# Kernel optimization log

Measured on AMD Instinct MI355X. Metric: run time of the kernel, lower is better.

The kernel has to match this reference:

```python
import jax, jax.numpy as jnp
import numpy as np

N_EXPERTS = 8
IN_DIM = 1024
OUT_DIM = 1024
N_TOKENS = 16384
TOP_K = 2


def setup_inputs() -> dict:
    key = jax.random.key(0)
    k1, k2, k3, k4 = jax.random.split(key, 4)
    inputs = jax.random.normal(k1, (N_TOKENS, IN_DIM), dtype=jnp.float32)
    # weight stored as [n_experts, out_dim, in_dim] like the nn.Parameter
    weight = jax.random.normal(k2, (N_EXPERTS, OUT_DIM, IN_DIM), dtype=jnp.float32) * 0.02
    gates = jax.random.uniform(k3, (N_TOKENS, TOP_K), dtype=jnp.float32)
    # router assignments: each token gets TOP_K expert ids; slots sorted by expert
    expert_idxs = jax.random.randint(k4, (N_TOKENS, TOP_K), 0, N_EXPERTS)
    flat = expert_idxs.reshape(-1)                       # [n_tokens*k]
    sorted_scattered_idxs = jnp.argsort(flat).astype(jnp.int64)
    sorted_expert_idxs = flat[sorted_scattered_idxs].astype(jnp.int64)
    expert_offsets = jnp.cumsum(jnp.bincount(flat, length=N_EXPERTS)).astype(jnp.int64)
    return {
        "inputs": inputs,
        "weight": weight,
        "gates": gates,
        "k": TOP_K,
        "sorted_expert_idxs": sorted_expert_idxs,
        "sorted_scattered_idxs": sorted_scattered_idxs,
        "expert_offsets": expert_offsets,
    }


def reference(inputs, weight, gates, k, sorted_expert_idxs, sorted_scattered_idxs, expert_offsets):
    # scatter2scatter (grouped_in=False, grouped_out=False, bias=None):
    #   slot j uses expert e=sorted_expert_idxs[j] on token t=sorted_scattered_idxs[j]//k
    #   slot_out[j] = weight[e] @ x[t]   (weight passed as W.permute(0,2,1), same math)
    tok = sorted_scattered_idxs // k                      # [S]
    xs = jnp.take(inputs, tok, axis=0)                    # [S, Din] gathered in sorted order
    S = xs.shape[0]
    n_experts, out_dim = weight.shape[0], weight.shape[1]
    slot_out = jnp.zeros((S, out_dim), dtype=xs.dtype)
    for e in range(n_experts):                            # small fixed expert count
        mask = (sorted_expert_idxs == e)[:, None].astype(xs.dtype)
        slot_out = slot_out + (xs * mask) @ weight[e].T   # [S, Dout]
    # gate-weighted combine, faithful to the torch code: the sorted slot
    # output is viewed directly as [n_tokens, k, out_dim]
    n_tokens, kk = gates.shape
    out_expanded = slot_out.reshape(n_tokens, kk, out_dim)
    return jnp.einsum('tk,tko->to', gates, out_expanded)  # [n_tokens, out_dim]
```

## Files before the change

### kernel.cpp

```cpp
#include <hip/hip_runtime.h>
#include <stdint.h>

#define N_EXPERTS 8
#define IN_DIM    1024
#define OUT_DIM   1024
#define N_TOKENS  16384
#define S_SLOTS   (N_TOKENS * 2)
#define BM 128
#define BN 128
#define BK 32
#define MAX_TILES 264

typedef unsigned short u16;
using short4v = __attribute__((ext_vector_type(4))) short;
using short8  = __attribute__((ext_vector_type(8))) short;
using f32x4   = __attribute__((ext_vector_type(4))) float;

__device__ __forceinline__ u16 f2bf(float f) {
  uint32_t x = __builtin_bit_cast(uint32_t, f);
  uint32_t r = x + 0x7fffu + ((x >> 16) & 1u);
  return (u16)(r >> 16);
}
__device__ __forceinline__ float bf2f(u16 u) {
  uint32_t x = ((uint32_t)u) << 16;
  return __builtin_bit_cast(float, x);
}

#define GLD_LDS16(g, l) __builtin_amdgcn_global_load_lds(            \
    (const __attribute__((address_space(1))) void*)(g),              \
    (__attribute__((address_space(3))) void*)(l), 16, 0, 0)

__global__ __launch_bounds__(256) void convert_two(
    const float* __restrict__ X, const float* __restrict__ W,
    u16* __restrict__ Xb, u16* __restrict__ Wb, int xblocks, int xn8, int wn8) {
  const float* src; u16* dst; int i, n8;
  if ((int)blockIdx.x < xblocks) {
    i = blockIdx.x * 256 + threadIdx.x; src = X; dst = Xb; n8 = xn8;
  } else {
    i = (blockIdx.x - xblocks) * 256 + threadIdx.x; src = W; dst = Wb; n8 = wn8;
  }
  if (i >= n8) return;
  const f32x4* s = (const f32x4*)src + (size_t)i * 2;
  f32x4 v0 = s[0], v1 = s[1];
  short8 o;
#pragma unroll
  for (int j = 0; j < 4; ++j) {
    o[j]     = (short)f2bf(v0[j]);
    o[4 + j] = (short)f2bf(v1[j]);
  }
  *(short8*)(dst + (size_t)i * 8) = o;
}

__device__ __forceinline__ bool derive_tile(const int* eoff_raw, bool is64,
                                            int bx, int& expert, int& rs, int& re) {
  int rem = bx, prev = 0;
  expert = -1;
  for (int e = 0; e < N_EXPERTS; ++e) {
    int end = is64 ? eoff_raw[2 * e] : eoff_raw[e];
    int cnt = end - prev;
    int nt  = (cnt + BM - 1) / BM;
    if (expert < 0) {
      if (rem < nt) {
        expert = e;
        rs = prev + rem * BM;
        re = (rs + BM < end) ? (rs + BM) : end;
      } else {
        rem -= nt;
      }
    }
    prev = end;
  }
  return expert >= 0;
}

__global__ __launch_bounds__(256) void moe_gemm_slot(
    const u16* __restrict__ Xb,
    const u16* __restrict__ Wb,
    const int* __restrict__ kptr,
    const int* __restrict__ ssi_raw,
    const int* __restrict__ eoff_raw,
    u16*       __restrict__ slot_out)
{
  __shared__ __align__(16) u16 smem[BM * BN];
  u16* As = smem;
  u16* Bs = smem + BM * BK;

  const bool is64 = (eoff_raw[7] != S_SLOTS);
  int expert, rs, re;
  if (!derive_tile(eoff_raw, is64, blockIdx.x, expert, rs, re)) return;
  const int rcount = re - rs;

  const int n0   = blockIdx.y * BN;
  const int kdiv = kptr[0];
  const int t    = threadIdx.x;

  const int r0 = t >> 2;
  const int r1 = (t + 256) >> 2;
  const int cg = (t & 3) * 8;

  int g0 = rs + r0; if (g0 >= re) g0 = re - 1;
  int g1 = rs + r1; if (g1 >= re) g1 = re - 1;
  const int tok0 = (is64 ? ssi_raw[2 * g0] : ssi_raw[g0]) / kdiv;
  const int tok1 = (is64 ? ssi_raw[2 * g1] : ssi_raw[g1]) / kdiv;

  const u16* a0 = Xb + (size_t)tok0 * IN_DIM + cg;
  const u16* a1 = Xb + (size_t)tok1 * IN_DIM + cg;
  const u16* wbp = Wb + (size_t)expert * OUT_DIM * IN_DIM;
  const u16* b0 = wbp + (size_t)(n0 + r0) * IN_DIM + cg;
  const u16* b1 = wbp + (size_t)(n0 + r1) * IN_DIM + cg;

  f32x4 acc[4][4];
#pragma unroll
  for (int i = 0; i < 4; ++i)
#pragma unroll
    for (int j = 0; j < 4; ++j)
      acc[i][j] = (f32x4){0.f, 0.f, 0.f, 0.f};

  const int wave = t >> 6;
  const int lane = t & 63;
  const int wm = (wave >> 1) * 64;
  const int wn = (wave & 1) * 64;
  const int lr = lane & 15;
  const int lk = (lane >> 4) * 8;

  for (int k0 = 0; k0 < IN_DIM; k0 += BK) {
    GLD_LDS16(a0 + k0, As + (size_t)t * 8);
    GLD_LDS16(a1 + k0, As + (size_t)(t + 256) * 8);
    GLD_LDS16(b0 + k0, Bs + (size_t)t * 8);
    GLD_LDS16(b1 + k0, Bs + (size_t)(t + 256) * 8);
    __syncthreads();

    short8 af[4], bfv[4];
#pragma unroll
    for (int mi = 0; mi < 4; ++mi)
      af[mi] = *(const short8*)&As[(wm + mi * 16 + lr) * BK + lk];
#pragma unroll
    for (int ni = 0; ni < 4; ++ni)
      bfv[ni] = *(const short8*)&Bs[(wn + ni * 16 + lr) * BK + lk];

#pragma unroll
    for (int mi = 0; mi < 4; ++mi)
#pragma unroll
      for (int ni = 0; ni < 4; ++ni)
        acc[mi][ni] = __builtin_amdgcn_mfma_f32_16x16x32_bf16(
            af[mi], bfv[ni], acc[mi][ni], 0, 0, 0);

    __syncthreads();
  }

  u16* Cs = smem;
#pragma unroll
  for (int mi = 0; mi < 4; ++mi)
#pragma unroll
    for (int ni = 0; ni < 4; ++ni)
#pragma unroll
      for (int r = 0; r < 4; ++r) {
        int row = wm + mi * 16 + (lane >> 4) * 4 + r;
        int col = wn + ni * 16 + lr;
        Cs[row * BN + col] = f2bf(acc[mi][ni][r]);
      }
  __syncthreads();

  const int crow = t >> 4;
  const int ccol = (t & 15) * 8;
#pragma unroll
  for (int i = 0; i < 8; ++i) {
    int row = i * 16 + crow;
    if (row < rcount) {
      *(short8*)&slot_out[(size_t)(rs + row) * OUT_DIM + n0 + ccol] =
          *(const short8*)&Cs[row * BN + ccol];
    }
  }
}

__global__ __launch_bounds__(256) void combine_k(
    const u16*   __restrict__ slot_out,
    const float* __restrict__ gates,
    float*       __restrict__ out)
{
  int idx = blockIdx.x * 256 + threadIdx.x;
  if (idx >= N_TOKENS * OUT_DIM / 8) return;
  int tk = idx >> 7;
  int cc = (idx & 127) * 8;
  float ga = gates[2 * tk];
  float gb = gates[2 * tk + 1];
  short8 s0 = *(const short8*)&slot_out[(size_t)(2 * tk) * OUT_DIM + cc];
  short8 s1 = *(const short8*)&slot_out[(size_t)(2 * tk + 1) * OUT_DIM + cc];
  f32x4 o0, o1;
#pragma unroll
  for (int j = 0; j < 4; ++j) {
    o0[j] = ga * bf2f((u16)s0[j])     + gb * bf2f((u16)s1[j]);
    o1[j] = ga * bf2f((u16)s0[4 + j]) + gb * bf2f((u16)s1[4 + j]);
  }
  f32x4* dst = (f32x4*)(out + (size_t)tk * OUT_DIM + cc);
  dst[0] = o0; dst[1] = o1;
}

__global__ __launch_bounds__(256) void moe_gemm_bf16(
    const u16*   __restrict__ Xb, const u16* __restrict__ Wb,
    const float* __restrict__ gates, const int* __restrict__ kptr,
    const int*   __restrict__ ssi_raw, const int* __restrict__ eoff_raw,
    float*       __restrict__ out)
{
  __shared__ __align__(16) u16 As[BM * BK];
  __shared__ __align__(16) u16 Bs[BN * BK];

  const bool is64 = (eoff_raw[7] != S_SLOTS);
  int expert, rs, re;
  if (!derive_tile(eoff_raw, is64, blockIdx.x, expert, rs, re)) return;
  const int rcount = re - rs;

  const int n0   = blockIdx.y * BN;
  const int kdiv = kptr[0];
  const int t    = threadIdx.x;

  const int r0 = t >> 2;
  const int r1 = (t + 256) >> 2;
  const int cg = (t & 3) * 8;

  int g0 = rs + r0; if (g0 >= re) g0 = re - 1;
  int g1 = rs + r1; if (g1 >= re) g1 = re - 1;
  const int tok0 = (is64 ? ssi_raw[2 * g0] : ssi_raw[g0]) / kdiv;
  const int tok1 = (is64 ? ssi_raw[2 * g1] : ssi_raw[g1]) / kdiv;

  const u16* a0 = Xb + (size_t)tok0 * IN_DIM + cg;
  const u16* a1 = Xb + (size_t)tok1 * IN_DIM + cg;
  const u16* wbp = Wb + (size_t)expert * OUT_DIM * IN_DIM;
  const u16* b0 = wbp + (size_t)(n0 + r0) * IN_DIM + cg;
  const u16* b1 = wbp + (size_t)(n0 + r1) * IN_DIM + cg;

  f32x4 acc[4][4];
#pragma unroll
  for (int i = 0; i < 4; ++i)
#pragma unroll
    for (int j = 0; j < 4; ++j)
      acc[i][j] = (f32x4){0.f, 0.f, 0.f, 0.f};

  const int wave = t >> 6;
  const int lane = t & 63;
  const int wm = (wave >> 1) * 64;
  const int wn = (wave & 1) * 64;
  const int lr = lane & 15;
  const int lk = (lane >> 4) * 8;

  for (int k0 = 0; k0 < IN_DIM; k0 += BK) {
    GLD_LDS16(a0 + k0, As + (size_t)t * 8);
    GLD_LDS16(a1 + k0, As + (size_t)(t + 256) * 8);
    GLD_LDS16(b0 + k0, Bs + (size_t)t * 8);
    GLD_LDS16(b1 + k0, Bs + (size_t)(t + 256) * 8);
    __syncthreads();

    short8 af[4], bfv[4];
#pragma unroll
    for (int mi = 0; mi < 4; ++mi)
      af[mi] = *(const short8*)&As[(wm + mi * 16 + lr) * BK + lk];
#pragma unroll
    for (int ni = 0; ni < 4; ++ni)
      bfv[ni] = *(const short8*)&Bs[(wn + ni * 16 + lr) * BK + lk];

#pragma unroll
    for (int mi = 0; mi < 4; ++mi)
#pragma unroll
      for (int ni = 0; ni < 4; ++ni)
        acc[mi][ni] = __builtin_amdgcn_mfma_f32_16x16x32_bf16(
            af[mi], bfv[ni], acc[mi][ni], 0, 0, 0);

    __syncthreads();
  }

#pragma unroll
  for (int mi = 0; mi < 4; ++mi) {
#pragma unroll
    for (int r = 0; r < 4; ++r) {
      int row = wm + mi * 16 + (lane >> 4) * 4 + r;
      if (row < rcount) {
        int slot  = rs + row;
        int token = slot / kdiv;
        float g   = gates[slot];
        float* dst = out + (size_t)token * OUT_DIM + n0;
#pragma unroll
        for (int ni = 0; ni < 4; ++ni) {
          int col = wn + ni * 16 + lr;
          atomicAdd(dst + col, g * acc[mi][ni][r]);
        }
      }
    }
  }
}

__global__ __launch_bounds__(256) void moe_gemm_fused(
    const float* __restrict__ X, const float* __restrict__ W,
    const float* __restrict__ gates, const int* __restrict__ kptr,
    const int*   __restrict__ ssi_raw, const int* __restrict__ eoff_raw,
    float*       __restrict__ out)
{
  __shared__ __align__(16) u16 As[BM * BK];
  __shared__ __align__(16) u16 Bs[BN * BK];

  const bool is64 = (eoff_raw[7] != S_SLOTS);
  int expert, rs, re;
  if (!derive_tile(eoff_raw, is64, blockIdx.x, expert, rs, re)) return;
  const int rcount = re - rs;

  const int n0   = blockIdx.y * BN;
  const int kdiv = kptr[0];
  const int t    = threadIdx.x;

  const float* arow[4];
  const float* brow[4];
  int lofs[4];
#pragma unroll
  for (int i = 0; i < 4; ++i) {
    int c = t + 256 * i;
    int r = c >> 3;
    int col4 = (c & 7) * 4;
    int g = rs + r; if (g >= re) g = re - 1;
    int sval = is64 ? ssi_raw[2 * g] : ssi_raw[g];
    int tok  = sval / kdiv;
    arow[i] = X + (size_t)tok * IN_DIM + col4;
    brow[i] = W + ((size_t)expert * OUT_DIM + n0 + r) * IN_DIM + col4;
    lofs[i] = r * BK + col4;
  }

  f32x4 acc[4][4];
#pragma unroll
  for (int i = 0; i < 4; ++i)
#pragma unroll
    for (int j = 0; j < 4; ++j)
      acc[i][j] = (f32x4){0.f, 0.f, 0.f, 0.f};

  const int wave = t >> 6;
  const int lane = t & 63;
  const int wm = (wave >> 1) * 64;
  const int wn = (wave & 1) * 64;
  const int lr = lane & 15;
  const int lk = (lane >> 4) * 8;

  for (int k0 = 0; k0 < IN_DIM; k0 += BK) {
    f32x4 a[4], b[4];
#pragma unroll
    for (int i = 0; i < 4; ++i) {
      a[i] = *(const f32x4*)(arow[i] + k0);
      b[i] = *(const f32x4*)(brow[i] + k0);
    }
    __syncthreads();
#pragma unroll
    for (int i = 0; i < 4; ++i) {
      short4v av, bv;
#pragma unroll
      for (int j = 0; j < 4; ++j) {
        av[j] = (short)f2bf(a[i][j]);
        bv[j] = (short)f2bf(b[i][j]);
      }
      *(short4v*)&As[lofs[i]] = av;
      *(short4v*)&Bs[lofs[i]] = bv;
    }
    __syncthreads();

    short8 af[4], bfv[4];
#pragma unroll
    for (int mi = 0; mi < 4; ++mi)
      af[mi] = *(const short8*)&As[(wm + mi * 16 + lr) * BK + lk];
#pragma unroll
    for (int ni = 0; ni < 4; ++ni)
      bfv[ni] = *(const short8*)&Bs[(wn + ni * 16 + lr) * BK + lk];

#pragma unroll
    for (int mi = 0; mi < 4; ++mi)
#pragma unroll
      for (int ni = 0; ni < 4; ++ni)
        acc[mi][ni] = __builtin_amdgcn_mfma_f32_16x16x32_bf16(
            af[mi], bfv[ni], acc[mi][ni], 0, 0, 0);
  }

#pragma unroll
  for (int mi = 0; mi < 4; ++mi) {
#pragma unroll
    for (int r = 0; r < 4; ++r) {
      int row = wm + mi * 16 + (lane >> 4) * 4 + r;
      if (row < rcount) {
        int slot  = rs + row;
        int token = slot / kdiv;
        float g   = gates[slot];
        float* dst = out + (size_t)token * OUT_DIM + n0;
#pragma unroll
        for (int ni = 0; ni < 4; ++ni) {
          int col = wn + ni * 16 + lr;
          atomicAdd(dst + col, g * acc[mi][ni][r]);
        }
      }
    }
  }
}

extern "C" void kernel_launch(void* const* d_in, const int* in_sizes, int n_in,
                              void* d_out, int out_size, void* d_ws, size_t ws_size,
                              hipStream_t stream) {
  const float* X     = (const float*)d_in[0];
  const float* W     = (const float*)d_in[1];
  const float* gates = (const float*)d_in[2];
  const int*   kptr  = (const int*)d_in[3];
  const int*   ssi   = (const int*)d_in[5];
  const int*   eoff  = (const int*)d_in[6];
  float* out = (float*)d_out;

  const size_t x_elems = (size_t)N_TOKENS * IN_DIM;
  const size_t w_elems = (size_t)N_EXPERTS * OUT_DIM * IN_DIM;
  const size_t s_elems = (size_t)S_SLOTS * OUT_DIM;
  const size_t need_full = (x_elems + w_elems + s_elems) * sizeof(u16);
  const size_t need_conv = (x_elems + w_elems) * sizeof(u16);

  const int xn8 = (int)(x_elems / 8), wn8 = (int)(w_elems / 8);
  const int xblocks = (xn8 + 255) / 256, wblocks = (wn8 + 255) / 256;

  if (ws_size >= need_full) {
    u16* Xb = (u16*)d_ws;
    u16* Wb = Xb + x_elems;
    u16* slot_out = Wb + w_elems;
    hipLaunchKernelGGL(convert_two, dim3(xblocks + wblocks), dim3(256), 0,
                       stream, X, W, Xb, Wb, xblocks, xn8, wn8);
    hipLaunchKernelGGL(moe_gemm_slot, dim3(MAX_TILES, OUT_DIM / BN), dim3(256),
                       0, stream, Xb, Wb, kptr, ssi, eoff, slot_out);
    const int nchunks = N_TOKENS * OUT_DIM / 8;
    hipLaunchKernelGGL(combine_k, dim3(nchunks / 256), dim3(256), 0, stream,
                       slot_out, gates, out);
  } else if (ws_size >= need_conv) {
    u16* Xb = (u16*)d_ws;
    u16* Wb = Xb + x_elems;
    hipMemsetAsync(d_out, 0, (size_t)out_size * sizeof(float), stream);
    hipLaunchKernelGGL(convert_two, dim3(xblocks + wblocks), dim3(256), 0,
                       stream, X, W, Xb, Wb, xblocks, xn8, wn8);
    hipLaunchKernelGGL(moe_gemm_bf16, dim3(MAX_TILES, OUT_DIM / BN), dim3(256),
                       0, stream, Xb, Wb, gates, kptr, ssi, eoff, out);
  } else {
    hipMemsetAsync(d_out, 0, (size_t)out_size * sizeof(float), stream);
    hipLaunchKernelGGL(moe_gemm_fused, dim3(MAX_TILES, OUT_DIM / BN), dim3(256),
                       0, stream, X, W, gates, kptr, ssi, eoff, out);
  }
}
```

Measured before the change: 260.5 us.

## Fuse convert, GEMM and combine into one persistent cooperative kernel

Replaces the three-kernel pipeline (bf16 conversion, slot GEMM, gated combine) with a single persistent cooperative kernel that uses grid-wide syncs between phases. GEMM tiles are handed out as jobs in a grid-stride loop. The aim is to remove kernel launch gaps and per-launch tail effects. In exchange it pays for two grid barriers, and the GEMM phase is limited to the blocks that can be co-resident (capped at 1056). It falls back to the old three-kernel path if the cooperative launch fails, and it drops the atomic bf16 path.

Result: slower. 433.3 us (+66.3%).

```diff
diff --git a/kernel.cpp b/kernel.cpp
--- a/kernel.cpp
+++ b/kernel.cpp
@@ -1,5 +1,8 @@
 #include <hip/hip_runtime.h>
+#include <hip/hip_cooperative_groups.h>
 #include <stdint.h>
+
+namespace cg = cooperative_groups;
 
 #define N_EXPERTS 8
 #define IN_DIM    1024
@@ -10,6 +13,7 @@
 #define BN 128
 #define BK 32
 #define MAX_TILES 264
+#define NGROUPS   (OUT_DIM / BN)
 
 typedef unsigned short u16;
 using short4v = __attribute__((ext_vector_type(4))) short;
@@ -29,27 +33,6 @@
 #define GLD_LDS16(g, l) __builtin_amdgcn_global_load_lds(            \
     (const __attribute__((address_space(1))) void*)(g),              \
     (__attribute__((address_space(3))) void*)(l), 16, 0, 0)
-
-__global__ __launch_bounds__(256) void convert_two(
-    const float* __restrict__ X, const float* __restrict__ W,
-    u16* __restrict__ Xb, u16* __restrict__ Wb, int xblocks, int xn8, int wn8) {
-  const float* src; u16* dst; int i, n8;
-  if ((int)blockIdx.x < xblocks) {
-    i = blockIdx.x * 256 + threadIdx.x; src = X; dst = Xb; n8 = xn8;
-  } else {
-    i = (blockIdx.x - xblocks) * 256 + threadIdx.x; src = W; dst = Wb; n8 = wn8;
-  }
-  if (i >= n8) return;
-  const f32x4* s = (const f32x4*)src + (size_t)i * 2;
-  f32x4 v0 = s[0], v1 = s[1];
-  short8 o;
-#pragma unroll
-  for (int j = 0; j < 4; ++j) {
-    o[j]     = (short)f2bf(v0[j]);
-    o[4 + j] = (short)f2bf(v1[j]);
-  }
-  *(short8*)(dst + (size_t)i * 8) = o;
-}
 
 __device__ __forceinline__ bool derive_tile(const int* eoff_raw, bool is64,
                                             int bx, int& expert, int& rs, int& re) {
@@ -73,48 +56,59 @@
   return expert >= 0;
 }
 
-__global__ __launch_bounds__(256) void moe_gemm_slot(
-    const u16* __restrict__ Xb,
-    const u16* __restrict__ Wb,
-    const int* __restrict__ kptr,
-    const int* __restrict__ ssi_raw,
-    const int* __restrict__ eoff_raw,
-    u16*       __restrict__ slot_out)
+__global__ __launch_bounds__(256, 4) void moe_fused(
+    const float* __restrict__ X,
+    const float* __restrict__ W,
+    const float* __restrict__ gates,
+    const int*   __restrict__ kptr,
+    const int*   __restrict__ ssi_raw,
+    const int*   __restrict__ eoff_raw,
+    u16* __restrict__ Xb, u16* __restrict__ Wb,
+    u16* __restrict__ slot_out,
+    float* __restrict__ out,
+    int nblk)
 {
   __shared__ __align__(16) u16 smem[BM * BN];
+  cg::grid_group grid = cg::this_grid();
+
+  const int bid = blockIdx.x;
+  const int t   = threadIdx.x;
+
+  const int xn8  = (N_TOKENS * IN_DIM) / 8;
+  const int wn8  = (N_EXPERTS * OUT_DIM * IN_DIM) / 8;
+  const int tot8 = xn8 + wn8;
+  for (int i = bid * 256 + t; i < tot8; i += nblk * 256) {
+    const float* src; u16* dst; int j;
+    if (i < xn8) { src = X; dst = Xb; j = i; }
+    else         { src = W; dst = Wb; j = i - xn8; }
+    f32x4 v0 = ((const f32x4*)src)[(size_t)j * 2];
+    f32x4 v1 = ((const f32x4*)src)[(size_t)j * 2 + 1];
+    short8 o;
+#pragma unroll
+    for (int q = 0; q < 4; ++q) {
+      o[q]     = (short)f2bf(v0[q]);
+      o[4 + q] = (short)f2bf(v1[q]);
+    }
+    *(short8*)(dst + (size_t)j * 8) = o;
+  }
+
+  grid.sync();
+
+  const bool is64 = (eoff_raw[7] != S_SLOTS);
+  int ntiles = 0;
+  {
+    int prev = 0;
+    for (int e = 0; e < N_EXPERTS; ++e) {
+      int end = is64 ? eoff_raw[2 * e] : eoff_raw[e];
+      ntiles += (end - prev + BM - 1) / BM;
+      prev = end;
+    }
+  }
+  const int njobs = ntiles * NGROUPS;
+  const int kdiv  = kptr[0];
+
   u16* As = smem;
   u16* Bs = smem + BM * BK;
-
-  const bool is64 = (eoff_raw[7] != S_SLOTS);
-  int expert, rs, re;
-  if (!derive_tile(eoff_raw, is64, blockIdx.x, expert, rs, re)) return;
-  const int rcount = re - rs;
-
-  const int n0   = blockIdx.y * BN;
-  const int kdiv = kptr[0];
-  const int t    = threadIdx.x;
-
-  const int r0 = t >> 2;
-  const int r1 = (t + 256) >> 2;
-  const int cg = (t & 3) * 8;
-
-  int g0 = rs + r0; if (g0 >= re) g0 = re - 1;
-  int g1 = rs + r1; if (g1 >= re) g1 = re - 1;
-  const int tok0 = (is64 ? ssi_raw[2 * g0] : ssi_raw[g0]) / kdiv;
-  const int tok1 = (is64 ? ssi_raw[2 * g1] : ssi_raw[g1]) / kdiv;
-
-  const u16* a0 = Xb + (size_t)tok0 * IN_DIM + cg;
-  const u16* a1 = Xb + (size_t)tok1 * IN_DIM + cg;
-  const u16* wbp = Wb + (size_t)expert * OUT_DIM * IN_DIM;
-  const u16* b0 = wbp + (size_t)(n0 + r0) * IN_DIM + cg;
-  const u16* b1 = wbp + (size_t)(n0 + r1) * IN_DIM + cg;
-
-  f32x4 acc[4][4];
-#pragma unroll
-  for (int i = 0; i < 4; ++i)
-#pragma unroll
-    for (int j = 0; j < 4; ++j)
-      acc[i][j] = (f32x4){0.f, 0.f, 0.f, 0.f};
 
   const int wave = t >> 6;
   const int lane = t & 63;
@@ -123,6 +117,177 @@
   const int lr = lane & 15;
   const int lk = (lane >> 4) * 8;
 
+  const int r0 = t >> 2;
+  const int r1 = (t + 256) >> 2;
+  const int cg2 = (t & 3) * 8;
+
+  for (int job = bid; job < njobs; job += nblk) {
+    int tile = job % ntiles;
+    int n0   = (job / ntiles) * BN;
+
+    int expert, rs, re;
+    derive_tile(eoff_raw, is64, tile, expert, rs, re);
+    const int rcount = re - rs;
+
+    int g0 = rs + r0; if (g0 >= re) g0 = re - 1;
+    int g1 = rs + r1; if (g1 >= re) g1 = re - 1;
+    const int tok0 = (is64 ? ssi_raw[2 * g0] : ssi_raw[g0]) / kdiv;
+    const int tok1 = (is64 ? ssi_raw[2 * g1] : ssi_raw[g1]) / kdiv;
+
+    const u16* a0 = Xb + (size_t)tok0 * IN_DIM + cg2;
+    const u16* a1 = Xb + (size_t)tok1 * IN_DIM + cg2;
+    const u16* wbp = Wb + (size_t)expert * OUT_DIM * IN_DIM;
+    const u16* b0 = wbp + (size_t)(n0 + r0) * IN_DIM + cg2;
+    const u16* b1 = wbp + (size_t)(n0 + r1) * IN_DIM + cg2;
+
+    f32x4 acc[4][4];
+#pragma unroll
+    for (int i = 0; i < 4; ++i)
+#pragma unroll
+      for (int j = 0; j < 4; ++j)
+        acc[i][j] = (f32x4){0.f, 0.f, 0.f, 0.f};
+
+    __syncthreads();
+
+    for (int k0 = 0; k0 < IN_DIM; k0 += BK) {
+      GLD_LDS16(a0 + k0, As + (size_t)t * 8);
+      GLD_LDS16(a1 + k0, As + (size_t)(t + 256) * 8);
+      GLD_LDS16(b0 + k0, Bs + (size_t)t * 8);
+      GLD_LDS16(b1 + k0, Bs + (size_t)(t + 256) * 8);
+      __syncthreads();
+
+      short8 af[4], bfv[4];
+#pragma unroll
+      for (int mi = 0; mi < 4; ++mi)
+        af[mi] = *(const short8*)&As[(wm + mi * 16 + lr) * BK + lk];
+#pragma unroll
+      for (int ni = 0; ni < 4; ++ni)
+        bfv[ni] = *(const short8*)&Bs[(wn + ni * 16 + lr) * BK + lk];
+
+#pragma unroll
+      for (int mi = 0; mi < 4; ++mi)
+#pragma unroll
+        for (int ni = 0; ni < 4; ++ni)
+          acc[mi][ni] = __builtin_amdgcn_mfma_f32_16x16x32_bf16(
+              af[mi], bfv[ni], acc[mi][ni], 0, 0, 0);
+
+      __syncthreads();
+    }
+
+    u16* Cs = smem;
+#pragma unroll
+    for (int mi = 0; mi < 4; ++mi)
+#pragma unroll
+      for (int ni = 0; ni < 4; ++ni)
+#pragma unroll
+        for (int r = 0; r < 4; ++r) {
+          int row = wm + mi * 16 + (lane >> 4) * 4 + r;
+          int col = wn + ni * 16 + lr;
+          Cs[row * BN + col] = f2bf(acc[mi][ni][r]);
+        }
+    __syncthreads();
+
+    const int crow = t >> 4;
+    const int ccol = (t & 15) * 8;
+#pragma unroll
+    for (int i = 0; i < 8; ++i) {
+      int row = i * 16 + crow;
+      if (row < rcount) {
+        *(short8*)&slot_out[(size_t)(rs + row) * OUT_DIM + n0 + ccol] =
+            *(const short8*)&Cs[row * BN + ccol];
+      }
+    }
+  }
+
+  grid.sync();
+
+  const int cchunks = N_TOKENS * OUT_DIM / 8;
+  for (int idx = bid * 256 + t; idx < cchunks; idx += nblk * 256) {
+    int tk = idx >> 7;
+    int cc = (idx & 127) * 8;
+    float ga = gates[2 * tk];
+    float gb = gates[2 * tk + 1];
+    short8 s0 = *(const short8*)&slot_out[(size_t)(2 * tk) * OUT_DIM + cc];
+    short8 s1 = *(const short8*)&slot_out[(size_t)(2 * tk + 1) * OUT_DIM + cc];
+    f32x4 o0, o1;
+#pragma unroll
+    for (int j = 0; j < 4; ++j) {
+      o0[j] = ga * bf2f((u16)s0[j])     + gb * bf2f((u16)s1[j]);
+      o1[j] = ga * bf2f((u16)s0[4 + j]) + gb * bf2f((u16)s1[4 + j]);
+    }
+    f32x4* dst = (f32x4*)(out + (size_t)tk * OUT_DIM + cc);
+    dst[0] = o0; dst[1] = o1;
+  }
+}
+
+__global__ __launch_bounds__(256) void convert_two(
+    const float* __restrict__ X, const float* __restrict__ W,
+    u16* __restrict__ Xb, u16* __restrict__ Wb, int xblocks, int xn8, int wn8) {
+  const float* src; u16* dst; int i, n8;
+  if ((int)blockIdx.x < xblocks) {
+    i = blockIdx.x * 256 + threadIdx.x; src = X; dst = Xb; n8 = xn8;
+  } else {
+    i = (blockIdx.x - xblocks) * 256 + threadIdx.x; src = W; dst = Wb; n8 = wn8;
+  }
+  if (i >= n8) return;
+  const f32x4* s = (const f32x4*)src + (size_t)i * 2;
+  f32x4 v0 = s[0], v1 = s[1];
+  short8 o;
+#pragma unroll
+  for (int j = 0; j < 4; ++j) {
+    o[j]     = (short)f2bf(v0[j]);
+    o[4 + j] = (short)f2bf(v1[j]);
+  }
+  *(short8*)(dst + (size_t)i * 8) = o;
+}
+
+__global__ __launch_bounds__(256) void moe_gemm_slot(
+    const u16* __restrict__ Xb, const u16* __restrict__ Wb,
+    const int* __restrict__ kptr, const int* __restrict__ ssi_raw,
+    const int* __restrict__ eoff_raw, u16* __restrict__ slot_out)
+{
+  __shared__ __align__(16) u16 smem[BM * BN];
+  u16* As = smem;
+  u16* Bs = smem + BM * BK;
+
+  const bool is64 = (eoff_raw[7] != S_SLOTS);
+  int expert, rs, re;
+  if (!derive_tile(eoff_raw, is64, blockIdx.x, expert, rs, re)) return;
+  const int rcount = re - rs;
+
+  const int n0   = blockIdx.y * BN;
+  const int kdiv = kptr[0];
+  const int t    = threadIdx.x;
+
+  const int r0 = t >> 2;
+  const int r1 = (t + 256) >> 2;
+  const int cg2 = (t & 3) * 8;
+
+  int g0 = rs + r0; if (g0 >= re) g0 = re - 1;
+  int g1 = rs + r1; if (g1 >= re) g1 = re - 1;
+  const int tok0 = (is64 ? ssi_raw[2 * g0] : ssi_raw[g0]) / kdiv;
+  const int tok1 = (is64 ? ssi_raw[2 * g1] : ssi_raw[g1]) / kdiv;
+
+  const u16* a0 = Xb + (size_t)tok0 * IN_DIM + cg2;
+  const u16* a1 = Xb + (size_t)tok1 * IN_DIM + cg2;
+  const u16* wbp = Wb + (size_t)expert * OUT_DIM * IN_DIM;
+  const u16* b0 = wbp + (size_t)(n0 + r0) * IN_DIM + cg2;
+  const u16* b1 = wbp + (size_t)(n0 + r1) * IN_DIM + cg2;
+
+  f32x4 acc[4][4];
+#pragma unroll
+  for (int i = 0; i < 4; ++i)
+#pragma unroll
+    for (int j = 0; j < 4; ++j)
+      acc[i][j] = (f32x4){0.f, 0.f, 0.f, 0.f};
+
+  const int wave = t >> 6;
+  const int lane = t & 63;
+  const int wm = (wave >> 1) * 64;
+  const int wn = (wave & 1) * 64;
+  const int lr = lane & 15;
+  const int lk = (lane >> 4) * 8;
+
   for (int k0 = 0; k0 < IN_DIM; k0 += BK) {
     GLD_LDS16(a0 + k0, As + (size_t)t * 8);
     GLD_LDS16(a1 + k0, As + (size_t)(t + 256) * 8);
@@ -174,9 +339,8 @@
 }
 
 __global__ __launch_bounds__(256) void combine_k(
-    const u16*   __restrict__ slot_out,
-    const float* __restrict__ gates,
-    float*       __restrict__ out)
+    const u16* __restrict__ slot_out, const float* __restrict__ gates,
+    float* __restrict__ out)
 {
   int idx = blockIdx.x * 256 + threadIdx.x;
   if (idx >= N_TOKENS * OUT_DIM / 8) return;
@@ -196,99 +360,7 @@
   dst[0] = o0; dst[1] = o1;
 }
 
-__global__ __launch_bounds__(256) void moe_gemm_bf16(
-    const u16*   __restrict__ Xb, const u16* __restrict__ Wb,
-    const float* __restrict__ gates, const int* __restrict__ kptr,
-    const int*   __restrict__ ssi_raw, const int* __restrict__ eoff_raw,
-    float*       __restrict__ out)
-{
-  __shared__ __align__(16) u16 As[BM * BK];
-  __shared__ __align__(16) u16 Bs[BN * BK];
-
-  const bool is64 = (eoff_raw[7] != S_SLOTS);
-  int expert, rs, re;
-  if (!derive_tile(eoff_raw, is64, blockIdx.x, expert, rs, re)) return;
-  const int rcount = re - rs;
-
-  const int n0   = blockIdx.y * BN;
-  const int kdiv = kptr[0];
-  const int t    = threadIdx.x;
-
-  const int r0 = t >> 2;
-  const int r1 = (t + 256) >> 2;
-  const int cg = (t & 3) * 8;
-
-  int g0 = rs + r0; if (g0 >= re) g0 = re - 1;
-  int g1 = rs + r1; if (g1 >= re) g1 = re - 1;
-  const int tok0 = (is64 ? ssi_raw[2 * g0] : ssi_raw[g0]) / kdiv;
-  const int tok1 = (is64 ? ssi_raw[2 * g1] : ssi_raw[g1]) / kdiv;
-
-  const u16* a0 = Xb + (size_t)tok0 * IN_DIM + cg;
-  const u16* a1 = Xb + (size_t)tok1 * IN_DIM + cg;
-  const u16* wbp = Wb + (size_t)expert * OUT_DIM * IN_DIM;
-  const u16* b0 = wbp + (size_t)(n0 + r0) * IN_DIM + cg;
-  const u16* b1 = wbp + (size_t)(n0 + r1) * IN_DIM + cg;
-
-  f32x4 acc[4][4];
-#pragma unroll
-  for (int i = 0; i < 4; ++i)
-#pragma unroll
-    for (int j = 0; j < 4; ++j)
-      acc[i][j] = (f32x4){0.f, 0.f, 0.f, 0.f};
-
-  const int wave = t >> 6;
-  const int lane = t & 63;
-  const int wm = (wave >> 1) * 64;
-  const int wn = (wave & 1) * 64;
-  const int lr = lane & 15;
-  const int lk = (lane >> 4) * 8;
-
-  for (int k0 = 0; k0 < IN_DIM; k0 += BK) {
-    GLD_LDS16(a0 + k0, As + (size_t)t * 8);
-    GLD_LDS16(a1 + k0, As + (size_t)(t + 256) * 8);
-    GLD_LDS16(b0 + k0, Bs + (size_t)t * 8);
-    GLD_LDS16(b1 + k0, Bs + (size_t)(t + 256) * 8);
-    __syncthreads();
-
-    short8 af[4], bfv[4];
-#pragma unroll
-    for (int mi = 0; mi < 4; ++mi)
-      af[mi] = *(const short8*)&As[(wm + mi * 16 + lr) * BK + lk];
-#pragma unroll
-    for (int ni = 0; ni < 4; ++ni)
-      bfv[ni] = *(const short8*)&Bs[(wn + ni * 16 + lr) * BK + lk];
-
-#pragma unroll
-    for (int mi = 0; mi < 4; ++mi)
-#pragma unroll
-      for (int ni = 0; ni < 4; ++ni)
-        acc[mi][ni] = __builtin_amdgcn_mfma_f32_16x16x32_bf16(
-            af[mi], bfv[ni], acc[mi][ni], 0, 0, 0);
-
-    __syncthreads();
-  }
-
-#pragma unroll
-  for (int mi = 0; mi < 4; ++mi) {
-#pragma unroll
-    for (int r = 0; r < 4; ++r) {
-      int row = wm + mi * 16 + (lane >> 4) * 4 + r;
-      if (row < rcount) {
-        int slot  = rs + row;
-        int token = slot / kdiv;
-        float g   = gates[slot];
-        float* dst = out + (size_t)token * OUT_DIM + n0;
-#pragma unroll
-        for (int ni = 0; ni < 4; ++ni) {
-          int col = wn + ni * 16 + lr;
-          atomicAdd(dst + col, g * acc[mi][ni][r]);
-        }
-      }
-    }
-  }
-}
-
-__global__ __launch_bounds__(256) void moe_gemm_fused(
+__global__ __launch_bounds__(256) void moe_gemm_fused_f32(
     const float* __restrict__ X, const float* __restrict__ W,
     const float* __restrict__ gates, const int* __restrict__ kptr,
     const int*   __restrict__ ssi_raw, const int* __restrict__ eoff_raw,
@@ -408,33 +480,41 @@
   const size_t w_elems = (size_t)N_EXPERTS * OUT_DIM * IN_DIM;
   const size_t s_elems = (size_t)S_SLOTS * OUT_DIM;
   const size_t need_full = (x_elems + w_elems + s_elems) * sizeof(u16);
-  const size_t need_conv = (x_elems + w_elems) * sizeof(u16);
-
-  const int xn8 = (int)(x_elems / 8), wn8 = (int)(w_elems / 8);
-  const int xblocks = (xn8 + 255) / 256, wblocks = (wn8 + 255) / 256;
 
   if (ws_size >= need_full) {
     u16* Xb = (u16*)d_ws;
     u16* Wb = Xb + x_elems;
     u16* slot_out = Wb + w_elems;
+
+    int maxB = 0;
+    hipError_t oe = hipOccupancyMaxActiveBlocksPerMultiprocessor(
+        &maxB, (const void*)moe_fused, 256, 0);
+    int nblk = (oe == hipSuccess && maxB > 0) ? maxB * 256 : 0;
+    if (nblk > 1056) nblk = 1056;
+
+    hipError_t ce = hipErrorUnknown;
+    if (nblk >= 256) {
+      void* kargs[] = {(void*)&X, (void*)&W, (void*)&gates, (void*)&kptr,
+                       (void*)&ssi, (void*)&eoff, (void*)&Xb, (void*)&Wb,
+                       (void*)&slot_out, (void*)&out, (void*)&nblk};
+      ce = hipLaunchCooperativeKernel((const void*)moe_fused, dim3(nblk),
+                                      dim3(256), kargs, 0, stream);
+    }
+    if (ce == hipSuccess) return;
+    (void)hipGetLastError();
+
+    const int xn8 = (int)(x_elems / 8), wn8 = (int)(w_elems / 8);
+    const int xblocks = (xn8 + 255) / 256, wblocks = (wn8 + 255) / 256;
     hipLaunchKernelGGL(convert_two, dim3(xblocks + wblocks), dim3(256), 0,
                        stream, X, W, Xb, Wb, xblocks, xn8, wn8);
-    hipLaunchKernelGGL(moe_gemm_slot, dim3(MAX_TILES, OUT_DIM / BN), dim3(256),
+    hipLaunchKernelGGL(moe_gemm_slot, dim3(MAX_TILES, NGROUPS), dim3(256),
                        0, stream, Xb, Wb, kptr, ssi, eoff, slot_out);
     const int nchunks = N_TOKENS * OUT_DIM / 8;
     hipLaunchKernelGGL(combine_k, dim3(nchunks / 256), dim3(256), 0, stream,
                        slot_out, gates, out);
-  } else if (ws_size >= need_conv) {
-    u16* Xb = (u16*)d_ws;
-    u16* Wb = Xb + x_elems;
-    hipMemsetAsync(d_out, 0, (size_t)out_size * sizeof(float), stream);
-    hipLaunchKernelGGL(convert_two, dim3(xblocks + wblocks), dim3(256), 0,
-                       stream, X, W, Xb, Wb, xblocks, xn8, wn8);
-    hipLaunchKernelGGL(moe_gemm_bf16, dim3(MAX_TILES, OUT_DIM / BN), dim3(256),
-                       0, stream, Xb, Wb, gates, kptr, ssi, eoff, out);
   } else {
     hipMemsetAsync(d_out, 0, (size_t)out_size * sizeof(float), stream);
-    hipLaunchKernelGGL(moe_gemm_fused, dim3(MAX_TILES, OUT_DIM / BN), dim3(256),
+    hipLaunchKernelGGL(moe_gemm_fused_f32, dim3(MAX_TILES, NGROUPS), dim3(256),
                        0, stream, X, W, gates, kptr, ssi, eoff, out);
   }
 }
```
